# Kernel tuning notes

Hardware: AMD Instinct MI355X
Metric: run time of the kernel (lower is better)

## Reference

```python
import jax, jax.numpy as jnp
import numpy as np

N_HEAD, D_MODEL, D_HEAD = 16, 1024, 64
SEQ, BATCH = 1024, 8
SCALE = 1.0 / (D_HEAD ** 0.5)
LN_EPS = 1e-5


def setup_inputs() -> dict:
    key = jax.random.key(0)
    ks = jax.random.split(key, 16)
    dk = N_HEAD * D_HEAD  # == D_MODEL
    init_qkv = 1.0 / np.sqrt(D_MODEL)
    init_out = 1.0 / np.sqrt(dk)
    u = lambda k, shp, lo, hi: jax.random.uniform(k, shp, jnp.float32, lo, hi)
    inp = {
        'dec_inp': jax.random.normal(ks[0], (SEQ, BATCH, D_MODEL), jnp.float32),
        'attn_mask': jnp.triu(jnp.ones((SEQ, SEQ), dtype=bool), k=1),  # causal
        'query_mean': u(ks[1], (dk, D_MODEL), -init_qkv, init_qkv),
        'key_mean': u(ks[2], (dk, D_MODEL), -init_qkv, init_qkv),
        'value_mean': u(ks[3], (dk, D_MODEL), -init_qkv, init_qkv),
        'query_std': u(ks[4], (dk, D_MODEL), 2 * np.log(init_qkv), np.log(init_qkv)),
        'key_std': u(ks[5], (dk, D_MODEL), 2 * np.log(init_qkv), np.log(init_qkv)),
        'value_std': u(ks[6], (dk, D_MODEL), 2 * np.log(init_qkv), np.log(init_qkv)),
        'output_mean': u(ks[7], (D_MODEL, dk), -init_out, init_out),
        'output_std': u(ks[8], (D_MODEL, dk), 2 * np.log(init_out), np.log(init_out)),
        'ln_gamma': jnp.ones((D_MODEL,), jnp.float32),
        'ln_beta': jnp.zeros((D_MODEL,), jnp.float32),
        # per-forward reparameterization noise (training mode)
        'eps_q': jax.random.normal(ks[9], (dk, D_MODEL), jnp.float32),
        'eps_k': jax.random.normal(ks[10], (dk, D_MODEL), jnp.float32),
        'eps_v': jax.random.normal(ks[11], (dk, D_MODEL), jnp.float32),
        'eps_o': jax.random.normal(ks[12], (D_MODEL, dk), jnp.float32),
    }
    return inp


def _forward(dec_inp, query_mean, key_mean, value_mean, query_std, key_std,
             value_std, output_mean, output_std, ln_gamma, ln_beta,
             eps_q, eps_k, eps_v, eps_o, attn_mask):
    S, B, _ = dec_inp.shape
    # Bayesian weight sampling: w = mean + eps * exp(std)
    qw = query_mean + eps_q * jnp.exp(query_std)
    kw = key_mean + eps_k * jnp.exp(key_std)
    vw = value_mean + eps_v * jnp.exp(value_std)
    # NOTE: original code (bug kept for faithfulness) builds the output weight
    # from value_mean + output_diff, not output_mean.
    ow = value_mean + eps_o * jnp.exp(output_std)

    head_q = (dec_inp @ qw.T).reshape(S, B, N_HEAD, D_HEAD)
    head_k = (dec_inp @ kw.T).reshape(S, B, N_HEAD, D_HEAD)
    head_v = (dec_inp @ vw.T).reshape(S, B, N_HEAD, D_HEAD)

    score = jnp.einsum('ibnd,jbnd->ijbn', head_q, head_k) * SCALE
    score = jnp.where(attn_mask[:, :, None, None], -jnp.inf, score)
    prob = jax.nn.softmax(score, axis=1)  # softmax over j (key) axis
    attn_vec = jnp.einsum('ijbn,jbnd->ibnd', prob, head_v).reshape(S, B, N_HEAD * D_HEAD)

    attn_out = attn_vec @ ow.T
    x = dec_inp + attn_out
    mu = jnp.mean(x, axis=-1, keepdims=True)
    var = jnp.var(x, axis=-1, keepdims=True)
    output = (x - mu) * jax.lax.rsqrt(var + LN_EPS) * ln_gamma + ln_beta

    theta_mean = jnp.concatenate([query_mean, key_mean, value_mean, output_mean.T], -1)
    theta_std = jnp.concatenate([query_std, key_std, value_std, output_std.T], -1)
    kl = jnp.mean(theta_mean ** 2 - theta_std * 2.0 + jnp.exp(theta_std * 2.0)) / 2.0
    return output, kl


def reference(dec_inp, attn_mask, query_mean, key_mean, value_mean, query_std,
              key_std, value_std, output_mean, output_std, ln_gamma, ln_beta,
              eps_q, eps_k, eps_v, eps_o):
    return _forward(dec_inp, query_mean, key_mean, value_mean, query_std,
                    key_std, value_std, output_mean, output_std, ln_gamma,
                    ln_beta, eps_q, eps_k, eps_v, eps_o, attn_mask)
```

## Files before the change

kernel.cpp:

```cpp
#include <hip/hip_runtime.h>

typedef _Float16 f16x8 __attribute__((ext_vector_type(8)));
typedef _Float16 f16x4 __attribute__((ext_vector_type(4)));
typedef float    f32x4 __attribute__((ext_vector_type(4)));

static __device__ __forceinline__ f32x4 mfma16(f16x8 a, f16x8 b, f32x4 c) {
    return __builtin_amdgcn_mfma_f32_16x16x32_f16(a, b, c, 0, 0, 0);
}

static __device__ __forceinline__ void gload_lds16(const _Float16* g, _Float16* lds) {
    __builtin_amdgcn_global_load_lds(
        (const __attribute__((address_space(1))) unsigned int*)g,
        (__attribute__((address_space(3))) unsigned int*)lds, 16, 0, 0);
}

__global__ __launch_bounds__(256) void k_prep(
    const float* __restrict__ qm, const float* __restrict__ km, const float* __restrict__ vm,
    const float* __restrict__ qs, const float* __restrict__ ks, const float* __restrict__ vs,
    const float* __restrict__ om, const float* __restrict__ os,
    const float* __restrict__ eq, const float* __restrict__ ek,
    const float* __restrict__ ev, const float* __restrict__ eo,
    _Float16* __restrict__ wq, _Float16* __restrict__ wk,
    _Float16* __restrict__ wv, _Float16* __restrict__ wo,
    float* __restrict__ part,
    const float* __restrict__ dec, _Float16* __restrict__ xh)
{
    if (blockIdx.x >= 1024) {
        int i = ((blockIdx.x - 1024) * 256 + threadIdx.x) * 4;
        float4 v = *(const float4*)&dec[i];
        f16x4 hv;
        hv[0] = (_Float16)v.x; hv[1] = (_Float16)v.y;
        hv[2] = (_Float16)v.z; hv[3] = (_Float16)v.w;
        *(f16x4*)&xh[i] = hv;
        return;
    }
    int i = (blockIdx.x * 256 + threadIdx.x) * 4;
    f32x4 aqm = *(const f32x4*)&qm[i], akm = *(const f32x4*)&km[i], avm = *(const f32x4*)&vm[i];
    f32x4 aqs = *(const f32x4*)&qs[i], aks = *(const f32x4*)&ks[i], avs = *(const f32x4*)&vs[i];
    f32x4 aom = *(const f32x4*)&om[i], aos = *(const f32x4*)&os[i];
    f32x4 veq = *(const f32x4*)&eq[i], vek = *(const f32x4*)&ek[i];
    f32x4 vev = *(const f32x4*)&ev[i], veo = *(const f32x4*)&eo[i];
    f16x4 hq, hk, hv, ho;
    float t = 0.f;
    #pragma unroll
    for (int j = 0; j < 4; ++j) {
        hq[j] = (_Float16)(aqm[j] + veq[j] * __expf(aqs[j]));
        hk[j] = (_Float16)(akm[j] + vek[j] * __expf(aks[j]));
        hv[j] = (_Float16)(avm[j] + vev[j] * __expf(avs[j]));
        ho[j] = (_Float16)(avm[j] + veo[j] * __expf(aos[j]));
        t += aqm[j]*aqm[j] - 2.f*aqs[j] + __expf(2.f*aqs[j])
           + akm[j]*akm[j] - 2.f*aks[j] + __expf(2.f*aks[j])
           + avm[j]*avm[j] - 2.f*avs[j] + __expf(2.f*avs[j])
           + aom[j]*aom[j] - 2.f*aos[j] + __expf(2.f*aos[j]);
    }
    *(f16x4*)&wq[i] = hq;
    *(f16x4*)&wk[i] = hk;
    *(f16x4*)&wv[i] = hv;
    *(f16x4*)&wo[i] = ho;
    #pragma unroll
    for (int m = 1; m < 64; m <<= 1) t += __shfl_xor(t, m, 64);
    __shared__ float red[4];
    int w = threadIdx.x >> 6, lane = threadIdx.x & 63;
    if (lane == 0) red[w] = t;
    __syncthreads();
    if (threadIdx.x == 0) part[blockIdx.x] = red[0] + red[1] + red[2] + red[3];
}

__global__ __launch_bounds__(256) void k_gemm(
    const _Float16* __restrict__ A, const _Float16* __restrict__ B0,
    _Float16* __restrict__ C0, const float* __restrict__ resid,
    float* __restrict__ xout, int mode)
{
    __shared__ __align__(16) _Float16 As[128 * 64];
    __shared__ __align__(16) _Float16 Bs[128 * 64];
    const int K = 1024, N = 1024;
    const _Float16* Bp = B0 + (size_t)blockIdx.z * 1048576u;
    _Float16* Cp = C0 + (size_t)blockIdx.z * 8388608u;
    int flat = blockIdx.y * 8 + blockIdx.x;
    int xcd = flat & 7, j = flat >> 3;
    int tM = (xcd * 8 + (j & 7)) * 128;
    int tN = (j >> 3) * 128;
    int tid = threadIdx.x, w = tid >> 6, lane = tid & 63;
    int wm = w & 1, wn = w >> 1;
    int q = lane >> 4, r = lane & 15;
    int csrc = ((lane & 7) ^ (lane >> 3)) * 8;
    int srow = lane >> 3;
    f32x4 acc[4][4] = {};
    for (int kk = 0; kk < K; kk += 64) {
        __syncthreads();
        #pragma unroll
        for (int i = 0; i < 4; ++i) {
            int chunk = w * 4 + i;
            int row = chunk * 8 + srow;
            gload_lds16(A  + (size_t)(tM + row) * K + kk + csrc, &As[chunk * 512]);
            gload_lds16(Bp + (size_t)(tN + row) * K + kk + csrc, &Bs[chunk * 512]);
        }
        __syncthreads();
        #pragma unroll
        for (int kc = 0; kc < 2; ++kc) {
            f16x8 af[4], bf[4];
            #pragma unroll
            for (int m = 0; m < 4; ++m) {
                int row = wm*64 + m*16 + r;
                int pos = ((kc*4 + q) ^ (r & 7)) * 8;
                af[m] = *(const f16x8*)&As[row*64 + pos];
            }
            #pragma unroll
            for (int n = 0; n < 4; ++n) {
                int row = wn*64 + n*16 + r;
                int pos = ((kc*4 + q) ^ (r & 7)) * 8;
                bf[n] = *(const f16x8*)&Bs[row*64 + pos];
            }
            #pragma unroll
            for (int m = 0; m < 4; ++m)
                #pragma unroll
                for (int n = 0; n < 4; ++n)
                    acc[m][n] = mfma16(af[m], bf[n], acc[m][n]);
        }
    }
    float sc = (mode == 0 && blockIdx.z == 0) ? 0.125f : 1.0f;
    #pragma unroll
    for (int m = 0; m < 4; ++m)
      #pragma unroll
      for (int n = 0; n < 4; ++n)
        #pragma unroll
        for (int t = 0; t < 4; ++t) {
            int row = tM + wm*64 + m*16 + q*4 + t;
            int col = tN + wn*64 + n*16 + r;
            size_t o = (size_t)row * N + col;
            if (mode == 0) Cp[o] = (_Float16)(acc[m][n][t] * sc);
            else           xout[o] = resid[o] + acc[m][n][t];
        }
}

__global__ __launch_bounds__(256) void k_vtrans(const _Float16* __restrict__ V,
                                                _Float16* __restrict__ Vt)
{
    __shared__ __align__(16) _Float16 L[64 * 72];
    int c = blockIdx.x;
    int b = c >> 4, h = c & 15;
    int s0 = blockIdx.y * 64;
    int tid = threadIdx.x;
    #pragma unroll
    for (int rep = 0; rep < 2; ++rep) {
        int idx = rep * 256 + tid;
        int sl = idx >> 3, ch = idx & 7;
        f16x8 v = *(const f16x8*)&V[((size_t)(s0 + sl) * 8 + b) * 1024 + h * 64 + ch * 8];
        *(f16x8*)&L[sl * 72 + ch * 8] = v;
    }
    __syncthreads();
    #pragma unroll
    for (int rep = 0; rep < 2; ++rep) {
        int idx = rep * 256 + tid;
        int d = idx >> 3, c2 = idx & 7;
        f16x8 o;
        #pragma unroll
        for (int e = 0; e < 8; ++e) o[e] = L[(c2 * 8 + e) * 72 + d];
        *(f16x8*)&Vt[((size_t)c * 64 + d) * 1024 + s0 + c2 * 8] = o;
    }
}

__global__ __launch_bounds__(256, 3) void k_attn(
    const _Float16* __restrict__ Qb, const _Float16* __restrict__ Kb,
    const _Float16* __restrict__ Vtg, _Float16* __restrict__ AVo)
{
    __shared__ __align__(16) _Float16 Ks[2][64 * 64];
    __shared__ __align__(16) _Float16 Vs[2][64 * 64];
    __shared__ __align__(16) _Float16 Ps[4 * 32 * 72];
    const int bh = blockIdx.x;
    const int b = bh & 7, h = bh >> 3;
    const int cbh = b * 16 + h;
    const int qt = (0x15623740u >> (blockIdx.y * 4)) & 7;
    const int tid = threadIdx.x, w = tid >> 6, lane = tid & 63;
    const int q = lane >> 4, r = lane & 15;
    const int i0 = qt * 128 + w * 32;
    const int csrc = ((lane & 7) ^ (lane >> 3)) * 8;
    const int srow = lane >> 3;

    f16x8 qf[2][2];
    #pragma unroll
    for (int it = 0; it < 2; ++it)
      #pragma unroll
      for (int kc = 0; kc < 2; ++kc)
        qf[it][kc] = *(const f16x8*)&Qb[((size_t)(i0 + it*16 + r)*8 + b)*1024 + h*64 + kc*32 + q*8];

    f32x4 ot[4][2] = {};
    float mrun[2] = {-1e30f, -1e30f}, lrun[2] = {0.f, 0.f};
    _Float16* Pw = &Ps[w * 2304];

    auto stage = [&](int kt, int buf) __attribute__((always_inline)) {
        #pragma unroll
        for (int ii = 0; ii < 2; ++ii) {
            int chunk = w * 2 + ii;
            int row = chunk * 8 + srow;
            gload_lds16(Kb  + ((size_t)(kt*64 + row)*8 + b)*1024 + h*64 + csrc, &Ks[buf][chunk*512]);
            gload_lds16(Vtg + ((size_t)(cbh*64 + row))*1024 + kt*64 + csrc,     &Vs[buf][chunk*512]);
        }
    };

    auto tile = [&](int kt, int buf, bool MASK) __attribute__((always_inline)) {
        f32x4 st[4][2] = {};
        #pragma unroll
        for (int kc = 0; kc < 2; ++kc) {
            f16x8 kf[4];
            #pragma unroll
            for (int jt = 0; jt < 4; ++jt) {
                int pos = ((kc*4 + q) ^ (r & 7)) * 8;
                kf[jt] = *(const f16x8*)&Ks[buf][(jt*16 + r)*64 + pos];
            }
            #pragma unroll
            for (int jt = 0; jt < 4; ++jt)
              #pragma unroll
              for (int it = 0; it < 2; ++it)
                st[jt][it] = mfma16(kf[jt], qf[it][kc], st[jt][it]);
        }

        #pragma unroll
        for (int it = 0; it < 2; ++it) {
            if (MASK) {
                int il = i0 + it*16 + r;
                #pragma unroll
                for (int jt = 0; jt < 4; ++jt)
                  #pragma unroll
                  for (int t = 0; t < 4; ++t)
                    if (kt*64 + jt*16 + q*4 + t > il) st[jt][it][t] = -1e30f;
            }
            float mx = -1e30f;
            #pragma unroll
            for (int jt = 0; jt < 4; ++jt) {
                f32x4 s4 = st[jt][it];
                mx = fmaxf(mx, fmaxf(fmaxf(s4[0], s4[1]), fmaxf(s4[2], s4[3])));
            }
            mx = fmaxf(mx, __shfl_xor(mx, 16, 64));
            mx = fmaxf(mx, __shfl_xor(mx, 32, 64));
            float mnew = fmaxf(mrun[it], mx);
            float al = __expf(mrun[it] - mnew);
            mrun[it] = mnew;
            float ps = 0.f;
            #pragma unroll
            for (int jt = 0; jt < 4; ++jt) {
                f16x4 hv;
                #pragma unroll
                for (int t = 0; t < 4; ++t) {
                    float e = __expf(st[jt][it][t] - mnew);
                    ps += e;
                    hv[t] = (_Float16)e;
                }
                *(f16x4*)&Pw[(it*16 + r)*72 + jt*16 + q*4] = hv;
            }
            ps += __shfl_xor(ps, 16, 64);
            ps += __shfl_xor(ps, 32, 64);
            lrun[it] = lrun[it] * al + ps;
            #pragma unroll
            for (int dtb = 0; dtb < 4; ++dtb) ot[dtb][it] *= al;
        }

        #pragma unroll
        for (int kc = 0; kc < 2; ++kc) {
            f16x8 vf[4], pf[2];
            #pragma unroll
            for (int dtb = 0; dtb < 4; ++dtb) {
                int pos = ((kc*4 + q) ^ (r & 7)) * 8;
                vf[dtb] = *(const f16x8*)&Vs[buf][(dtb*16 + r)*64 + pos];
            }
            #pragma unroll
            for (int it = 0; it < 2; ++it)
                pf[it] = *(const f16x8*)&Pw[(it*16 + r)*72 + kc*32 + q*8];
            #pragma unroll
            for (int dtb = 0; dtb < 4; ++dtb)
              #pragma unroll
              for (int it = 0; it < 2; ++it)
                ot[dtb][it] = mfma16(vf[dtb], pf[it], ot[dtb][it]);
        }
    };

    stage(0, 0);
    __syncthreads();
    for (int kt = 0; kt < 2*qt; ++kt) {
        stage(kt + 1, (kt + 1) & 1);
        tile(kt, kt & 1, false);
        __syncthreads();
    }
    {
        int kt = 2*qt;
        stage(kt + 1, (kt + 1) & 1);
        tile(kt, kt & 1, true);
        __syncthreads();
        tile(kt + 1, (kt + 1) & 1, true);
    }

    #pragma unroll
    for (int it = 0; it < 2; ++it) {
        float inv = 1.f / lrun[it];
        int s = i0 + it*16 + r;
        #pragma unroll
        for (int dtb = 0; dtb < 4; ++dtb) {
            f16x4 hv;
            #pragma unroll
            for (int t = 0; t < 4; ++t) hv[t] = (_Float16)(ot[dtb][it][t] * inv);
            *(f16x4*)&AVo[((size_t)s*8 + b)*1024 + h*64 + dtb*16 + q*4] = hv;
        }
    }
}

__global__ __launch_bounds__(256) void k_ln(float* __restrict__ x,
    const float* __restrict__ g, const float* __restrict__ bta,
    const float* __restrict__ part)
{
    __shared__ float rs[4], rs2[4];
    int w = threadIdx.x >> 6, lane = threadIdx.x & 63;
    if (blockIdx.x == 8192) {
        float s = 0.f;
        for (int i = threadIdx.x; i < 1024; i += 256) s += part[i];
        #pragma unroll
        for (int m = 1; m < 64; m <<= 1) s += __shfl_xor(s, m, 64);
        if (lane == 0) rs[w] = s;
        __syncthreads();
        if (threadIdx.x == 0)
            x[8388608] = (rs[0] + rs[1] + rs[2] + rs[3]) * (0.5f / 4194304.f);
        return;
    }
    int row = blockIdx.x;
    float* xr = x + (size_t)row * 1024;
    int t4 = threadIdx.x * 4;
    float4 v = *(const float4*)&xr[t4];
    float s  = v.x + v.y + v.z + v.w;
    float s2 = v.x*v.x + v.y*v.y + v.z*v.z + v.w*v.w;
    #pragma unroll
    for (int m = 1; m < 64; m <<= 1) { s += __shfl_xor(s, m, 64); s2 += __shfl_xor(s2, m, 64); }
    if (lane == 0) { rs[w] = s; rs2[w] = s2; }
    __syncthreads();
    s  = rs[0] + rs[1] + rs[2] + rs[3];
    s2 = rs2[0] + rs2[1] + rs2[2] + rs2[3];
    float mu = s * (1.f / 1024.f);
    float var = s2 * (1.f / 1024.f) - mu * mu;
    float rstd = rsqrtf(var + 1e-5f);
    float4 gv = *(const float4*)&g[t4];
    float4 bv = *(const float4*)&bta[t4];
    float4 ov;
    ov.x = (v.x - mu) * rstd * gv.x + bv.x;
    ov.y = (v.y - mu) * rstd * gv.y + bv.y;
    ov.z = (v.z - mu) * rstd * gv.z + bv.z;
    ov.w = (v.w - mu) * rstd * gv.w + bv.w;
    *(float4*)&xr[t4] = ov;
}

extern "C" void kernel_launch(void* const* d_in, const int* in_sizes, int n_in,
                              void* d_out, int out_size, void* d_ws, size_t ws_size,
                              hipStream_t stream)
{
    (void)in_sizes; (void)n_in; (void)out_size; (void)ws_size;
    const float* dec   = (const float*)d_in[0];
    const float* qm    = (const float*)d_in[2];
    const float* km    = (const float*)d_in[3];
    const float* vm    = (const float*)d_in[4];
    const float* qs    = (const float*)d_in[5];
    const float* ks    = (const float*)d_in[6];
    const float* vs    = (const float*)d_in[7];
    const float* om    = (const float*)d_in[8];
    const float* os    = (const float*)d_in[9];
    const float* gamma = (const float*)d_in[10];
    const float* beta  = (const float*)d_in[11];
    const float* eq    = (const float*)d_in[12];
    const float* ek    = (const float*)d_in[13];
    const float* ev    = (const float*)d_in[14];
    const float* eo    = (const float*)d_in[15];

    char* ws = (char*)d_ws;
    _Float16* WQ   = (_Float16*)ws;
    float*    PART = (float*)(ws + (8ull  << 20));
    _Float16* XH   = (_Float16*)(ws + (9ull  << 20));
    _Float16* Qh   = (_Float16*)(ws + (25ull << 20));
    _Float16* Kh   = Qh + 8388608;
    _Float16* Vh   = Qh + 16777216;
    _Float16* Vtg  = XH;
    _Float16* AV   = Vh;
    float*    out  = (float*)d_out;

    k_prep<<<dim3(9216), dim3(256), 0, stream>>>(
        qm, km, vm, qs, ks, vs, om, os, eq, ek, ev, eo,
        WQ, WQ + 1048576, WQ + 2097152, WQ + 3145728, PART, dec, XH);
    k_gemm<<<dim3(8, 64, 3), dim3(256), 0, stream>>>(XH, WQ, Qh, dec, out, 0);
    k_vtrans<<<dim3(128, 16), dim3(256), 0, stream>>>(Vh, Vtg);
    k_attn<<<dim3(128, 8), dim3(256), 0, stream>>>(Qh, Kh, Vtg, AV);
    k_gemm<<<dim3(8, 64, 1), dim3(256), 0, stream>>>(AV, WQ + 3145728, Qh, dec, out, 1);
    k_ln<<<dim3(8193), dim3(256), 0, stream>>>(out, gamma, beta, PART);
}
```

Baseline: 308.4 us.

## Double-buffer GEMM LDS, add MFMA priority hints, lazy softmax rescale

The projection GEMM now uses two LDS buffers and prefetches the next K-slice while computing the current one, removing one barrier per iteration and overlapping global loads with MFMA work. The attention kernel wraps its MFMA blocks in s_setprio so waves issuing matrix ops get scheduling priority. It also skips the online-softmax rescale of the accumulators unless the running max grows by more than 8 in some lane. Doubling LDS in the GEMM may lower occupancy, and the lazy rescale lets exponentials reach up to e^8, which could cost fp16 precision in P.

```diff
diff --git a/kernel.cpp b/kernel.cpp
--- a/kernel.cpp
+++ b/kernel.cpp
@@ -71,8 +71,8 @@
     _Float16* __restrict__ C0, const float* __restrict__ resid,
     float* __restrict__ xout, int mode)
 {
-    __shared__ __align__(16) _Float16 As[128 * 64];
-    __shared__ __align__(16) _Float16 Bs[128 * 64];
+    __shared__ __align__(16) _Float16 As[2][128 * 64];
+    __shared__ __align__(16) _Float16 Bs[2][128 * 64];
     const int K = 1024, N = 1024;
     const _Float16* Bp = B0 + (size_t)blockIdx.z * 1048576u;
     _Float16* Cp = C0 + (size_t)blockIdx.z * 8388608u;
@@ -85,17 +85,24 @@
     int q = lane >> 4, r = lane & 15;
     int csrc = ((lane & 7) ^ (lane >> 3)) * 8;
     int srow = lane >> 3;
-    f32x4 acc[4][4] = {};
-    for (int kk = 0; kk < K; kk += 64) {
-        __syncthreads();
+
+    auto stage = [&](int t, int buf) __attribute__((always_inline)) {
+        int kk = t * 64;
         #pragma unroll
         for (int i = 0; i < 4; ++i) {
             int chunk = w * 4 + i;
             int row = chunk * 8 + srow;
-            gload_lds16(A  + (size_t)(tM + row) * K + kk + csrc, &As[chunk * 512]);
-            gload_lds16(Bp + (size_t)(tN + row) * K + kk + csrc, &Bs[chunk * 512]);
-        }
-        __syncthreads();
+            gload_lds16(A  + (size_t)(tM + row) * K + kk + csrc, &As[buf][chunk * 512]);
+            gload_lds16(Bp + (size_t)(tN + row) * K + kk + csrc, &Bs[buf][chunk * 512]);
+        }
+    };
+
+    f32x4 acc[4][4] = {};
+    stage(0, 0);
+    __syncthreads();
+    for (int t = 0; t < 16; ++t) {
+        const int cur = t & 1;
+        if (t < 15) stage(t + 1, cur ^ 1);
         #pragma unroll
         for (int kc = 0; kc < 2; ++kc) {
             f16x8 af[4], bf[4];
@@ -103,13 +110,13 @@
             for (int m = 0; m < 4; ++m) {
                 int row = wm*64 + m*16 + r;
                 int pos = ((kc*4 + q) ^ (r & 7)) * 8;
-                af[m] = *(const f16x8*)&As[row*64 + pos];
+                af[m] = *(const f16x8*)&As[cur][row*64 + pos];
             }
             #pragma unroll
             for (int n = 0; n < 4; ++n) {
                 int row = wn*64 + n*16 + r;
                 int pos = ((kc*4 + q) ^ (r & 7)) * 8;
-                bf[n] = *(const f16x8*)&Bs[row*64 + pos];
+                bf[n] = *(const f16x8*)&Bs[cur][row*64 + pos];
             }
             #pragma unroll
             for (int m = 0; m < 4; ++m)
@@ -117,7 +124,9 @@
                 for (int n = 0; n < 4; ++n)
                     acc[m][n] = mfma16(af[m], bf[n], acc[m][n]);
         }
-    }
+        __syncthreads();
+    }
+
     float sc = (mode == 0 && blockIdx.z == 0) ? 0.125f : 1.0f;
     #pragma unroll
     for (int m = 0; m < 4; ++m)
@@ -208,11 +217,13 @@
                 int pos = ((kc*4 + q) ^ (r & 7)) * 8;
                 kf[jt] = *(const f16x8*)&Ks[buf][(jt*16 + r)*64 + pos];
             }
+            __builtin_amdgcn_s_setprio(1);
             #pragma unroll
             for (int jt = 0; jt < 4; ++jt)
               #pragma unroll
               for (int it = 0; it < 2; ++it)
                 st[jt][it] = mfma16(kf[jt], qf[it][kc], st[jt][it]);
+            __builtin_amdgcn_s_setprio(0);
         }
 
         #pragma unroll
@@ -233,16 +244,22 @@
             }
             mx = fmaxf(mx, __shfl_xor(mx, 16, 64));
             mx = fmaxf(mx, __shfl_xor(mx, 32, 64));
-            float mnew = fmaxf(mrun[it], mx);
-            float al = __expf(mrun[it] - mnew);
-            mrun[it] = mnew;
+            if (!__all(mx - mrun[it] <= 8.f)) {
+                float mnew = fmaxf(mrun[it], mx);
+                float al = __expf(mrun[it] - mnew);
+                lrun[it] *= al;
+                #pragma unroll
+                for (int dtb = 0; dtb < 4; ++dtb) ot[dtb][it] *= al;
+                mrun[it] = mnew;
+            }
+            float mref = mrun[it];
             float ps = 0.f;
             #pragma unroll
             for (int jt = 0; jt < 4; ++jt) {
                 f16x4 hv;
                 #pragma unroll
                 for (int t = 0; t < 4; ++t) {
-                    float e = __expf(st[jt][it][t] - mnew);
+                    float e = __expf(st[jt][it][t] - mref);
                     ps += e;
                     hv[t] = (_Float16)e;
                 }
@@ -250,9 +267,7 @@
             }
             ps += __shfl_xor(ps, 16, 64);
             ps += __shfl_xor(ps, 32, 64);
-            lrun[it] = lrun[it] * al + ps;
-            #pragma unroll
-            for (int dtb = 0; dtb < 4; ++dtb) ot[dtb][it] *= al;
+            lrun[it] += ps;
         }
 
         #pragma unroll
@@ -266,11 +281,13 @@
             #pragma unroll
             for (int it = 0; it < 2; ++it)
                 pf[it] = *(const f16x8*)&Pw[(it*16 + r)*72 + kc*32 + q*8];
+            __builtin_amdgcn_s_setprio(1);
             #pragma unroll
             for (int dtb = 0; dtb < 4; ++dtb)
               #pragma unroll
               for (int it = 0; it < 2; ++it)
                 ot[dtb][it] = mfma16(vf[dtb], pf[it], ot[dtb][it]);
+            __builtin_amdgcn_s_setprio(0);
         }
     };
 
```

After: 308.6 us. No clear change (+0.1%).
